# Optimization experiments

Measured on AMD Instinct MI355X. Metric: run time of the kernel, lower is better.

The kernel has to match this reference:

```python
import jax, jax.numpy as jnp
import numpy as np
import math

D_MODEL = 512
NHEAD = 8
D_HEAD = D_MODEL // NHEAD
D_FF = 2048
N_LAYERS = 6
B, S = 8, 2048
EPS = 1e-5


def _layernorm(x, g, b):
    mu = jnp.mean(x, axis=-1, keepdims=True)
    var = jnp.mean(jnp.square(x - mu), axis=-1, keepdims=True)
    return (x - mu) * jax.lax.rsqrt(var + EPS) * g + b


def setup_inputs() -> dict:
    key = jax.random.key(0)
    ks = jax.random.split(key, 10)
    sc = 1.0 / math.sqrt(D_MODEL)
    scf = 1.0 / math.sqrt(D_FF)
    return {
        "x": jax.random.normal(ks[0], (B, S, D_MODEL), jnp.float32),
        "wq": jax.random.normal(ks[1], (N_LAYERS, D_MODEL, D_MODEL), jnp.float32) * sc,
        "wk": jax.random.normal(ks[2], (N_LAYERS, D_MODEL, D_MODEL), jnp.float32) * sc,
        "wv": jax.random.normal(ks[3], (N_LAYERS, D_MODEL, D_MODEL), jnp.float32) * sc,
        "wo": jax.random.normal(ks[4], (N_LAYERS, D_MODEL, D_MODEL), jnp.float32) * sc,
        "w1": jax.random.normal(ks[5], (N_LAYERS, D_MODEL, D_FF), jnp.float32) * sc,
        "b1": jnp.zeros((N_LAYERS, D_FF), jnp.float32),
        "w2": jax.random.normal(ks[6], (N_LAYERS, D_FF, D_MODEL), jnp.float32) * scf,
        "b2": jnp.zeros((N_LAYERS, D_MODEL), jnp.float32),
        "g1": jnp.ones((N_LAYERS, D_MODEL), jnp.float32),
        "beta1": jnp.zeros((N_LAYERS, D_MODEL), jnp.float32),
        "g2": jnp.ones((N_LAYERS, D_MODEL), jnp.float32),
        "beta2": jnp.zeros((N_LAYERS, D_MODEL), jnp.float32),
    }


def reference(x, wq, wk, wv, wo, w1, b1, w2, b2, g1, beta1, g2, beta2):
    scale = 1.0 / math.sqrt(D_HEAD)
    for i in range(N_LAYERS):
        # NOTE: faithful to torch .view(B, nhead, -1, d_head) WITHOUT transpose
        q = (x @ wq[i]).reshape(B, NHEAD, S, D_HEAD)
        k = (x @ wk[i]).reshape(B, NHEAD, S, D_HEAD)
        v = (x @ wv[i]).reshape(B, NHEAD, S, D_HEAD)
        u = jnp.einsum("bhsd,bhtd->bhst", q, k) * scale
        attn = jax.nn.softmax(u, axis=-1)
        o = jnp.einsum("bhst,bhtd->bhsd", attn, v).reshape(B, S, D_MODEL)
        x = _layernorm(x + o @ wo[i], g1[i], beta1[i])
        f = jax.nn.relu(x @ w1[i] + b1[i]) @ w2[i] + b2[i]
        x = _layernorm(x + f, g2[i], beta2[i])
    return x
```

## Files before the change

kernel.cpp:

```cpp
#include <hip/hip_runtime.h>
#include <hip/hip_bf16.h>
#include <stdint.h>

typedef __bf16 bf16_t;
typedef bf16_t bf16x8 __attribute__((ext_vector_type(8)));
typedef bf16_t bf16x4 __attribute__((ext_vector_type(4)));
typedef float  f32x4  __attribute__((ext_vector_type(4)));

#define AS1 __attribute__((address_space(1)))
#define AS3 __attribute__((address_space(3)))

__device__ __forceinline__ void gload_lds16(const void* g, void* l) {
  __builtin_amdgcn_global_load_lds((const AS1 void*)g, (AS3 void*)l, 16, 0, 0);
}

__device__ __forceinline__ float fast_exp2(float x) {
#if __has_builtin(__builtin_amdgcn_exp2f)
  return __builtin_amdgcn_exp2f(x);
#else
  return exp2f(x);
#endif
}

#define QSCALE 0.1803368801111204f

template <int RELU, int BIAS, int QKV, int DBUF>
__global__ __launch_bounds__(256) void gemm_bt(const bf16_t* __restrict__ A,
                                               const bf16_t* __restrict__ Bt,
                                               const float* __restrict__ bias,
                                               bf16_t* __restrict__ Cv,
                                               int M, int N, int K, int ldc) {
  __shared__ __align__(16) char smem[DBUF ? 65536 : 32768];
  const int t = threadIdx.x;
  const int l = t & 63;
  const int w = t >> 6;
  const int wm = w >> 1, wn = w & 1;
  const int lr = l & 15, lg = l >> 4;

  const int gx = gridDim.x;
  const int nwg = gx * gridDim.y;
  const int orig = blockIdx.y * gx + blockIdx.x;
  const int swz = (orig & 7) * (nwg >> 3) + (orig >> 3);
  const long m0 = (long)(swz / gx) * 128;
  const long n0 = (long)(swz % gx) * 128;

  const bf16_t* asrc[4];
  const bf16_t* bsrc[4];
#pragma unroll
  for (int it = 0; it < 4; ++it) {
    int y = it * 4096 + t * 16;
    int row = y >> 7;
    int col = ((y & 127) ^ ((row & 7) << 4)) >> 1;
    asrc[it] = A + (m0 + row) * (long)K + col;
    bsrc[it] = Bt + (n0 + row) * (long)K + col;
  }

  auto stage = [&](int buf) {
    char* sb = smem + buf * 32768;
#pragma unroll
    for (int it = 0; it < 4; ++it) {
      gload_lds16(asrc[it], sb + it * 4096 + t * 16);
      gload_lds16(bsrc[it], sb + 16384 + it * 4096 + t * 16);
      asrc[it] += 64;
      bsrc[it] += 64;
    }
  };

  f32x4 acc[4][4] = {};
  const int nt = K >> 6;

  auto compute = [&](char* sb) {
#pragma unroll
    for (int kk = 0; kk < 2; ++kk) {
      const int c2 = (kk * 32 + lg * 8) * 2;
      bf16x8 a[4], b[4];
#pragma unroll
      for (int i = 0; i < 4; ++i) {
        int ra = wm * 64 + i * 16 + lr;
        a[i] = *(const bf16x8*)(sb + ((ra * 128 + c2) ^ ((ra & 7) << 4)));
        int rb = wn * 64 + i * 16 + lr;
        b[i] = *(const bf16x8*)(sb + 16384 + ((rb * 128 + c2) ^ ((rb & 7) << 4)));
      }
      __builtin_amdgcn_s_setprio(1);
#pragma unroll
      for (int i = 0; i < 4; ++i)
#pragma unroll
        for (int j = 0; j < 4; ++j)
          acc[i][j] = __builtin_amdgcn_mfma_f32_16x16x32_bf16(a[i], b[j], acc[i][j], 0, 0, 0);
      __builtin_amdgcn_s_setprio(0);
    }
  };

  if (DBUF) {
    stage(0);
    __syncthreads();
    int buf = 0;
    for (int kt = 0; kt < nt; ++kt) {
      if (kt + 1 < nt) stage(buf ^ 1);
      compute(smem + buf * 32768);
      __syncthreads();
      buf ^= 1;
    }
  } else {
    for (int kt = 0; kt < nt; ++kt) {
      __syncthreads();
      stage(0);
      __syncthreads();
      compute(smem);
    }
  }

  float bv[4];
  if (BIAS) {
#pragma unroll
    for (int j = 0; j < 4; ++j) bv[j] = bias[n0 + wn * 64 + j * 16 + lr];
  }
#pragma unroll
  for (int i = 0; i < 4; ++i) {
    long rowb = m0 + wm * 64 + i * 16 + lg * 4;
#pragma unroll
    for (int j = 0; j < 4; ++j) {
      int colbase = (int)n0 + wn * 64 + j * 16;
      bf16_t* outp;
      int coll;
      if (QKV) {
        outp = Cv + (size_t)(colbase >> 9) * 8388608;
        coll = (colbase & 511) + lr;
      } else {
        outp = Cv;
        coll = colbase + lr;
      }
#pragma unroll
      for (int r = 0; r < 4; ++r) {
        float v = acc[i][j][r];
        if (BIAS) v += bv[j];
        if (RELU) v = v > 0.f ? v : 0.f;
        outp[(rowb + r) * (long)ldc + coll] = (bf16_t)v;
      }
    }
  }
}

__global__ __launch_bounds__(256) void attn_fa(const bf16_t* __restrict__ qg,
                                               const bf16_t* __restrict__ kg,
                                               const bf16_t* __restrict__ vg,
                                               bf16_t* __restrict__ og) {
  __shared__ __align__(16) char smem[49152];
  const int t = threadIdx.x, l = t & 63, w = t >> 6;
  const int lr = l & 15, lg = l >> 4;
  const int lin = blockIdx.x;
  const int swz = (lin & 7) * 128 + (lin >> 3);
  const long hoff = (long)(swz >> 4) * 131072;
  const int q0 = (swz & 15) * 128 + w * 32;
  const uint32_t LDSB = (uint32_t)(uintptr_t)(AS3 char*)smem;

  bf16x8 qf[2][2];
#pragma unroll
  for (int nf = 0; nf < 2; ++nf)
#pragma unroll
    for (int kk = 0; kk < 2; ++kk)
      qf[nf][kk] = *(const bf16x8*)(qg + hoff + (long)(q0 + nf * 16 + lr) * 64 + kk * 32 + lg * 8);

  const bf16_t* ksrc[2];
#pragma unroll
  for (int i = 0; i < 2; ++i) {
    int y = i * 4096 + t * 16;
    int row = y >> 7;
    int col = ((y & 127) ^ ((row & 7) << 4)) >> 1;
    ksrc[i] = kg + hoff + (long)row * 64 + col;
  }
  const bf16_t* vsrc[2];
#pragma unroll
  for (int i = 0; i < 2; ++i) {
    int y = i * 4096 + t * 16;
    int kk = y >> 12;
    int nj = (y >> 10) & 3;
    int jhi = (y >> 9) & 1;
    int lgs = (y >> 7) & 3;
    int r = (y >> 5) & 3;
    int ch = (y >> 4) & 1;
    int kv = kk * 32 + jhi * 16 + lgs * 4 + r;
    int d0 = nj * 16 + ch * 8;
    vsrc[i] = vg + hoff + (long)kv * 64 + d0;
  }

  auto stage = [&](int buf) {
    char* sb = smem + buf * 16384;
    gload_lds16(ksrc[0], sb + t * 16);
    gload_lds16(ksrc[1], sb + 4096 + t * 16);
    gload_lds16(vsrc[0], sb + 8192 + t * 16);
    gload_lds16(vsrc[1], sb + 12288 + t * 16);
    ksrc[0] += 4096; ksrc[1] += 4096; vsrc[0] += 4096; vsrc[1] += 4096;
  };

  f32x4 oacc[2][4] = {};
  f32x4 lacc[2] = {};
  bf16x8 onesf;
#pragma unroll
  for (int j = 0; j < 8; ++j) onesf[j] = (bf16_t)1.0f;

  stage(0);
  stage(1);
  int cur = 0, nxt = 2;
  for (int ti = 0; ti < 32; ++ti) {
    if (ti == 31) asm volatile("s_waitcnt vmcnt(0)" ::: "memory");
    else          asm volatile("s_waitcnt vmcnt(4)" ::: "memory");
    asm volatile("s_barrier" ::: "memory");
    if (ti < 30) stage(nxt);
    char* sb = smem + cur * 16384;

    f32x4 sT[4][2] = {};
#pragma unroll
    for (int kk = 0; kk < 2; ++kk) {
      const int c2 = (kk * 32 + lg * 8) * 2;
      bf16x8 kf[4];
#pragma unroll
      for (int mf = 0; mf < 4; ++mf) {
        int rk = mf * 16 + lr;
        kf[mf] = *(const bf16x8*)(sb + ((rk * 128 + c2) ^ ((rk & 7) << 4)));
      }
      __builtin_amdgcn_s_setprio(1);
#pragma unroll
      for (int mf = 0; mf < 4; ++mf)
#pragma unroll
        for (int nf = 0; nf < 2; ++nf)
          sT[mf][nf] = __builtin_amdgcn_mfma_f32_16x16x32_bf16(kf[mf], qf[nf][kk], sT[mf][nf], 0, 0, 0);
      __builtin_amdgcn_s_setprio(0);
    }

    uint32_t va = LDSB + (uint32_t)cur * 16384u + 8192u + (uint32_t)l * 8u;
    bf16x4 tv0, tv1, tv2, tv3, tv4, tv5, tv6, tv7;
    bf16x4 tv8, tv9, tva, tvb, tvc, tvd, tve, tvf;
    asm volatile(
        "ds_read_b64_tr_b16 %0, %16 offset:0\n\t"
        "ds_read_b64_tr_b16 %1, %16 offset:512\n\t"
        "ds_read_b64_tr_b16 %2, %16 offset:1024\n\t"
        "ds_read_b64_tr_b16 %3, %16 offset:1536\n\t"
        "ds_read_b64_tr_b16 %4, %16 offset:2048\n\t"
        "ds_read_b64_tr_b16 %5, %16 offset:2560\n\t"
        "ds_read_b64_tr_b16 %6, %16 offset:3072\n\t"
        "ds_read_b64_tr_b16 %7, %16 offset:3584\n\t"
        "ds_read_b64_tr_b16 %8, %16 offset:4096\n\t"
        "ds_read_b64_tr_b16 %9, %16 offset:4608\n\t"
        "ds_read_b64_tr_b16 %10, %16 offset:5120\n\t"
        "ds_read_b64_tr_b16 %11, %16 offset:5632\n\t"
        "ds_read_b64_tr_b16 %12, %16 offset:6144\n\t"
        "ds_read_b64_tr_b16 %13, %16 offset:6656\n\t"
        "ds_read_b64_tr_b16 %14, %16 offset:7168\n\t"
        "ds_read_b64_tr_b16 %15, %16 offset:7680"
        : "=&v"(tv0), "=&v"(tv1), "=&v"(tv2), "=&v"(tv3),
          "=&v"(tv4), "=&v"(tv5), "=&v"(tv6), "=&v"(tv7),
          "=&v"(tv8), "=&v"(tv9), "=&v"(tva), "=&v"(tvb),
          "=&v"(tvc), "=&v"(tvd), "=&v"(tve), "=&v"(tvf)
        : "v"(va));

    bf16x8 pa[2][2];
#pragma unroll
    for (int m2 = 0; m2 < 2; ++m2)
#pragma unroll
      for (int kk = 0; kk < 2; ++kk) {
        f32x4 e0, e1;
#pragma unroll
        for (int r = 0; r < 4; ++r) {
          e0[r] = fast_exp2(sT[2 * kk][m2][r]);
          e1[r] = fast_exp2(sT[2 * kk + 1][m2][r]);
        }
        bf16x4 c0 = __builtin_convertvector(e0, bf16x4);
        bf16x4 c1 = __builtin_convertvector(e1, bf16x4);
        pa[m2][kk] = __builtin_shufflevector(c0, c1, 0, 1, 2, 3, 4, 5, 6, 7);
      }

    asm volatile("s_waitcnt lgkmcnt(0)" ::: "memory");
    __builtin_amdgcn_sched_barrier(0);

    bf16x8 vf[2][4];
    vf[0][0] = __builtin_shufflevector(tv0, tv1, 0, 1, 2, 3, 4, 5, 6, 7);
    vf[0][1] = __builtin_shufflevector(tv2, tv3, 0, 1, 2, 3, 4, 5, 6, 7);
    vf[0][2] = __builtin_shufflevector(tv4, tv5, 0, 1, 2, 3, 4, 5, 6, 7);
    vf[0][3] = __builtin_shufflevector(tv6, tv7, 0, 1, 2, 3, 4, 5, 6, 7);
    vf[1][0] = __builtin_shufflevector(tv8, tv9, 0, 1, 2, 3, 4, 5, 6, 7);
    vf[1][1] = __builtin_shufflevector(tva, tvb, 0, 1, 2, 3, 4, 5, 6, 7);
    vf[1][2] = __builtin_shufflevector(tvc, tvd, 0, 1, 2, 3, 4, 5, 6, 7);
    vf[1][3] = __builtin_shufflevector(tve, tvf, 0, 1, 2, 3, 4, 5, 6, 7);

    __builtin_amdgcn_s_setprio(1);
#pragma unroll
    for (int kk = 0; kk < 2; ++kk)
#pragma unroll
      for (int m2 = 0; m2 < 2; ++m2) {
#pragma unroll
        for (int nj = 0; nj < 4; ++nj)
          oacc[m2][nj] = __builtin_amdgcn_mfma_f32_16x16x32_bf16(pa[m2][kk], vf[kk][nj], oacc[m2][nj], 0, 0, 0);
        lacc[m2] = __builtin_amdgcn_mfma_f32_16x16x32_bf16(pa[m2][kk], onesf, lacc[m2], 0, 0, 0);
      }
    __builtin_amdgcn_s_setprio(0);

    cur = (cur == 2) ? 0 : cur + 1;
    nxt = (nxt == 2) ? 0 : nxt + 1;
  }

#pragma unroll
  for (int m2 = 0; m2 < 2; ++m2)
#pragma unroll
    for (int r = 0; r < 4; ++r) {
      float inv = 1.f / lacc[m2][r];
      long row = q0 + m2 * 16 + lg * 4 + r;
#pragma unroll
      for (int nj = 0; nj < 4; ++nj)
        og[hoff + row * 64 + nj * 16 + lr] = (bf16_t)(oacc[m2][nj][r] * inv);
    }
}

__global__ __launch_bounds__(256) void transpose_w(const float* __restrict__ src,
                                                   bf16_t* __restrict__ dst,
                                                   int K, int N,
                                                   long dstLayerStride, float scale) {
  __shared__ float tile[32][33];
  const int t = threadIdx.x;
  const int tx = t & 31, ty = t >> 5;
  const long ls = (long)blockIdx.z * K * N;
  const long ld = (long)blockIdx.z * dstLayerStride;
  const int n0 = blockIdx.x * 32, k0 = blockIdx.y * 32;
#pragma unroll
  for (int i = 0; i < 4; ++i)
    tile[ty + i * 8][tx] = src[ls + (long)(k0 + ty + i * 8) * N + n0 + tx];
  __syncthreads();
#pragma unroll
  for (int i = 0; i < 4; ++i)
    dst[ld + (long)(n0 + ty + i * 8) * K + k0 + tx] = (bf16_t)(tile[tx][ty + i * 8] * scale);
}

__global__ __launch_bounds__(256) void init_x(const float* __restrict__ x,
                                              bf16_t* __restrict__ xb) {
  long i = ((long)blockIdx.x * 256 + threadIdx.x) * 8;
  f32x4 a = *(const f32x4*)(x + i);
  f32x4 b = *(const f32x4*)(x + i + 4);
  bf16x8 o;
#pragma unroll
  for (int j = 0; j < 4; ++j) { o[j] = (bf16_t)a[j]; o[4 + j] = (bf16_t)b[j]; }
  *(bf16x8*)(xb + i) = o;
}

template <int FINAL>
__global__ __launch_bounds__(256) void resid_ln(const bf16_t* __restrict__ delta,
                                                bf16_t* __restrict__ xb,
                                                float* __restrict__ xout,
                                                const float* __restrict__ g,
                                                const float* __restrict__ b) {
  const int t = threadIdx.x, l = t & 63, w = t >> 6;
  const long row = (long)blockIdx.x * 4 + w;
  const long base = row * 512 + l * 8;
  bf16x8 xv = *(const bf16x8*)(xb + base);
  bf16x8 dv = *(const bf16x8*)(delta + base);
  float s[8];
  float sum = 0.f, sq = 0.f;
#pragma unroll
  for (int j = 0; j < 8; ++j) {
    s[j] = (float)xv[j] + (float)dv[j];
    sum += s[j];
    sq += s[j] * s[j];
  }
#pragma unroll
  for (int m = 1; m <= 32; m <<= 1) {
    sum += __shfl_xor(sum, m, 64);
    sq += __shfl_xor(sq, m, 64);
  }
  float mu = sum * (1.f / 512.f);
  float var = sq * (1.f / 512.f) - mu * mu;
  float rstd = rsqrtf(var + 1e-5f);
  f32x4 g0 = *(const f32x4*)(g + l * 8);
  f32x4 g1v = *(const f32x4*)(g + l * 8 + 4);
  f32x4 b0 = *(const f32x4*)(b + l * 8);
  f32x4 b1v = *(const f32x4*)(b + l * 8 + 4);
  f32x4 y0, y1;
  bf16x8 yb;
#pragma unroll
  for (int j = 0; j < 4; ++j) {
    y0[j] = (s[j] - mu) * rstd * g0[j] + b0[j];
    y1[j] = (s[4 + j] - mu) * rstd * g1v[j] + b1v[j];
    yb[j] = (bf16_t)y0[j];
    yb[4 + j] = (bf16_t)y1[j];
  }
  *(bf16x8*)(xb + base) = yb;
  if (FINAL) {
    *(f32x4*)(xout + base) = y0;
    *(f32x4*)(xout + base + 4) = y1;
  }
}

extern "C" void kernel_launch(void* const* d_in, const int* in_sizes, int n_in,
                              void* d_out, int out_size, void* d_ws, size_t ws_size,
                              hipStream_t stream) {
  const float* x = (const float*)d_in[0];
  const float* wq = (const float*)d_in[1];
  const float* wk = (const float*)d_in[2];
  const float* wv = (const float*)d_in[3];
  const float* wo = (const float*)d_in[4];
  const float* w1 = (const float*)d_in[5];
  const float* b1 = (const float*)d_in[6];
  const float* w2 = (const float*)d_in[7];
  const float* b2 = (const float*)d_in[8];
  const float* g1 = (const float*)d_in[9];
  const float* be1 = (const float*)d_in[10];
  const float* g2 = (const float*)d_in[11];
  const float* be2 = (const float*)d_in[12];

  char* ws = (char*)d_ws;

  const int M = 16384, D = 512, DFF = 2048, NL = 6;
  const size_t sz_small = (size_t)NL * D * D * 2;
  const size_t sz_big = (size_t)NL * D * DFF * 2;
  bf16_t* wqkvt = (bf16_t*)(ws);
  bf16_t* wot = (bf16_t*)(ws + 3 * sz_small);
  bf16_t* w1t = (bf16_t*)(ws + 4 * sz_small);
  bf16_t* w2t = (bf16_t*)(ws + 4 * sz_small + sz_big);
  char* actbase = ws + 4 * sz_small + 2 * sz_big;
  bf16_t* xb = (bf16_t*)(actbase);
  char* R = actbase + (size_t)M * D * 2;
  bf16_t* qb = (bf16_t*)(R);
  bf16_t* kb = (bf16_t*)(R + (size_t)M * D * 2);
  bf16_t* vb = (bf16_t*)(R + 2 * (size_t)M * D * 2);
  bf16_t* ob = (bf16_t*)(R + 3 * (size_t)M * D * 2);
  bf16_t* hb = (bf16_t*)(R);
  bf16_t* tmpb = (bf16_t*)(R + 4 * (size_t)M * D * 2);

  const long LQKV = 1536L * 512;
  transpose_w<<<dim3(D / 32, D / 32, NL), 256, 0, stream>>>(wq, wqkvt, D, D, LQKV, QSCALE);
  transpose_w<<<dim3(D / 32, D / 32, NL), 256, 0, stream>>>(wk, wqkvt + 512 * 512, D, D, LQKV, 1.f);
  transpose_w<<<dim3(D / 32, D / 32, NL), 256, 0, stream>>>(wv, wqkvt + 2 * 512 * 512, D, D, LQKV, 1.f);
  transpose_w<<<dim3(D / 32, D / 32, NL), 256, 0, stream>>>(wo, wot, D, D, (long)D * D, 1.f);
  transpose_w<<<dim3(DFF / 32, D / 32, NL), 256, 0, stream>>>(w1, w1t, D, DFF, (long)D * DFF, 1.f);
  transpose_w<<<dim3(D / 32, DFF / 32, NL), 256, 0, stream>>>(w2, w2t, DFF, D, (long)D * DFF, 1.f);
  init_x<<<4096, 256, 0, stream>>>(x, xb);

  for (int L = 0; L < NL; ++L) {
    const bf16_t* wqkvL = wqkvt + (size_t)L * LQKV;
    const bf16_t* woL = wot + (size_t)L * D * D;
    const bf16_t* w1L = w1t + (size_t)L * D * DFF;
    const bf16_t* w2L = w2t + (size_t)L * D * DFF;

    gemm_bt<0, 0, 1, 0><<<dim3(12, 128), 256, 0, stream>>>(xb, wqkvL, nullptr, qb, M, 1536, D, 512);
    attn_fa<<<dim3(1024), 256, 0, stream>>>(qb, kb, vb, ob);
    gemm_bt<0, 0, 0, 1><<<dim3(4, 128), 256, 0, stream>>>(ob, woL, nullptr, tmpb, M, D, D, D);
    resid_ln<0><<<4096, 256, 0, stream>>>(tmpb, xb, nullptr, g1 + L * D, be1 + L * D);
    gemm_bt<1, 1, 0, 0><<<dim3(16, 128), 256, 0, stream>>>(xb, w1L, b1 + (size_t)L * DFF, hb, M, DFF, D, DFF);
    gemm_bt<0, 1, 0, 1><<<dim3(4, 128), 256, 0, stream>>>(hb, w2L, b2 + L * D, tmpb, M, D, DFF, D);
    if (L == NL - 1)
      resid_ln<1><<<4096, 256, 0, stream>>>(tmpb, xb, (float*)d_out, g2 + L * D, be2 + L * D);
    else
      resid_ln<0><<<4096, 256, 0, stream>>>(tmpb, xb, nullptr, g2 + L * D, be2 + L * D);
  }
}
```

Baseline: 1.482 ms.

## Load K tiles directly into registers and stage only V through LDS

The attention kernel now reads K fragments straight from global memory into registers, double-buffered across iterations, instead of staging K through shared memory. Only V still goes through LDS, so shared memory per block shrinks from 48KB to 16KB with double buffering replacing the triple-buffered ring. This is meant to cut LDS traffic and footprint and allow more blocks per CU. In exchange it raises register pressure from holding two K fragment sets, and each lane now issues its own global K loads. The wait now drains all outstanding memory loads every iteration, which reduces how far prefetch can run ahead.

```diff
diff --git a/kernel.cpp b/kernel.cpp
--- a/kernel.cpp
+++ b/kernel.cpp
@@ -145,7 +145,7 @@
                                                const bf16_t* __restrict__ kg,
                                                const bf16_t* __restrict__ vg,
                                                bf16_t* __restrict__ og) {
-  __shared__ __align__(16) char smem[49152];
+  __shared__ __align__(16) char smem[16384];
   const int t = threadIdx.x, l = t & 63, w = t >> 6;
   const int lr = l & 15, lg = l >> 4;
   const int lin = blockIdx.x;
@@ -161,37 +161,17 @@
     for (int kk = 0; kk < 2; ++kk)
       qf[nf][kk] = *(const bf16x8*)(qg + hoff + (long)(q0 + nf * 16 + lr) * 64 + kk * 32 + lg * 8);
 
-  const bf16_t* ksrc[2];
-#pragma unroll
-  for (int i = 0; i < 2; ++i) {
-    int y = i * 4096 + t * 16;
-    int row = y >> 7;
-    int col = ((y & 127) ^ ((row & 7) << 4)) >> 1;
-    ksrc[i] = kg + hoff + (long)row * 64 + col;
-  }
-  const bf16_t* vsrc[2];
-#pragma unroll
-  for (int i = 0; i < 2; ++i) {
-    int y = i * 4096 + t * 16;
-    int kk = y >> 12;
+  const bf16_t* kbase = kg + hoff + (long)lr * 64 + lg * 8;
+  const bf16_t* vs;
+  {
+    int y = t * 16;
     int nj = (y >> 10) & 3;
     int jhi = (y >> 9) & 1;
     int lgs = (y >> 7) & 3;
     int r = (y >> 5) & 3;
     int ch = (y >> 4) & 1;
-    int kv = kk * 32 + jhi * 16 + lgs * 4 + r;
-    int d0 = nj * 16 + ch * 8;
-    vsrc[i] = vg + hoff + (long)kv * 64 + d0;
-  }
-
-  auto stage = [&](int buf) {
-    char* sb = smem + buf * 16384;
-    gload_lds16(ksrc[0], sb + t * 16);
-    gload_lds16(ksrc[1], sb + 4096 + t * 16);
-    gload_lds16(vsrc[0], sb + 8192 + t * 16);
-    gload_lds16(vsrc[1], sb + 12288 + t * 16);
-    ksrc[0] += 4096; ksrc[1] += 4096; vsrc[0] += 4096; vsrc[1] += 4096;
-  };
+    vs = vg + hoff + (long)(jhi * 16 + lgs * 4 + r) * 64 + nj * 16 + ch * 8;
+  }
 
   f32x4 oacc[2][4] = {};
   f32x4 lacc[2] = {};
@@ -199,36 +179,27 @@
 #pragma unroll
   for (int j = 0; j < 8; ++j) onesf[j] = (bf16_t)1.0f;
 
-  stage(0);
-  stage(1);
-  int cur = 0, nxt = 2;
-  for (int ti = 0; ti < 32; ++ti) {
-    if (ti == 31) asm volatile("s_waitcnt vmcnt(0)" ::: "memory");
-    else          asm volatile("s_waitcnt vmcnt(4)" ::: "memory");
+  bf16x8 kA[2][4], kB[2][4];
+
+  gload_lds16(vs, smem + t * 16);
+  gload_lds16(vs + 2048, smem + 4096 + t * 16);
+  vs += 4096;
+#pragma unroll
+  for (int kk = 0; kk < 2; ++kk)
+#pragma unroll
+    for (int mf = 0; mf < 4; ++mf)
+      kA[kk][mf] = *(const bf16x8*)(kbase + mf * 1024 + kk * 32);
+  kbase += 4096;
+
+  auto iter = [&](int buf, bf16x8 (&kf)[2][4], bool pre, int nbuf, bf16x8 (&kn)[2][4]) {
+    asm volatile("s_waitcnt vmcnt(0)" ::: "memory");
     asm volatile("s_barrier" ::: "memory");
-    if (ti < 30) stage(nxt);
-    char* sb = smem + cur * 16384;
-
-    f32x4 sT[4][2] = {};
-#pragma unroll
-    for (int kk = 0; kk < 2; ++kk) {
-      const int c2 = (kk * 32 + lg * 8) * 2;
-      bf16x8 kf[4];
-#pragma unroll
-      for (int mf = 0; mf < 4; ++mf) {
-        int rk = mf * 16 + lr;
-        kf[mf] = *(const bf16x8*)(sb + ((rk * 128 + c2) ^ ((rk & 7) << 4)));
-      }
-      __builtin_amdgcn_s_setprio(1);
-#pragma unroll
-      for (int mf = 0; mf < 4; ++mf)
-#pragma unroll
-        for (int nf = 0; nf < 2; ++nf)
-          sT[mf][nf] = __builtin_amdgcn_mfma_f32_16x16x32_bf16(kf[mf], qf[nf][kk], sT[mf][nf], 0, 0, 0);
-      __builtin_amdgcn_s_setprio(0);
-    }
-
-    uint32_t va = LDSB + (uint32_t)cur * 16384u + 8192u + (uint32_t)l * 8u;
+    if (pre) {
+      gload_lds16(vs, smem + nbuf * 8192 + t * 16);
+      gload_lds16(vs + 2048, smem + nbuf * 8192 + 4096 + t * 16);
+      vs += 4096;
+    }
+    uint32_t va = LDSB + (uint32_t)buf * 8192u + (uint32_t)l * 8u;
     bf16x4 tv0, tv1, tv2, tv3, tv4, tv5, tv6, tv7;
     bf16x4 tv8, tv9, tva, tvb, tvc, tvd, tve, tvf;
     asm volatile(
@@ -253,6 +224,25 @@
           "=&v"(tv8), "=&v"(tv9), "=&v"(tva), "=&v"(tvb),
           "=&v"(tvc), "=&v"(tvd), "=&v"(tve), "=&v"(tvf)
         : "v"(va));
+    if (pre) {
+#pragma unroll
+      for (int kk = 0; kk < 2; ++kk)
+#pragma unroll
+        for (int mf = 0; mf < 4; ++mf)
+          kn[kk][mf] = *(const bf16x8*)(kbase + mf * 1024 + kk * 32);
+      kbase += 4096;
+    }
+
+    f32x4 sT[4][2] = {};
+    __builtin_amdgcn_s_setprio(1);
+#pragma unroll
+    for (int kk = 0; kk < 2; ++kk)
+#pragma unroll
+      for (int mf = 0; mf < 4; ++mf)
+#pragma unroll
+        for (int nf = 0; nf < 2; ++nf)
+          sT[mf][nf] = __builtin_amdgcn_mfma_f32_16x16x32_bf16(kf[kk][mf], qf[nf][kk], sT[mf][nf], 0, 0, 0);
+    __builtin_amdgcn_s_setprio(0);
 
     bf16x8 pa[2][2];
 #pragma unroll
@@ -294,9 +284,12 @@
         lacc[m2] = __builtin_amdgcn_mfma_f32_16x16x32_bf16(pa[m2][kk], onesf, lacc[m2], 0, 0, 0);
       }
     __builtin_amdgcn_s_setprio(0);
-
-    cur = (cur == 2) ? 0 : cur + 1;
-    nxt = (nxt == 2) ? 0 : nxt + 1;
+  };
+
+  for (int ti = 0; ti < 32; ti += 2) {
+    iter(0, kA, true, 1, kB);
+    bool more = (ti + 2 < 32);
+    iter(1, kB, more, 0, kA);
   }
 
 #pragma unroll
```

Result: slower. 2.113 ms (+42.5%).

## Fuse output-projection and FFN2 GEMMs with residual add and LayerNorm

Applied to the files above, without the earlier changes.

Replaces the Wo and W2 GEMMs plus their separate resid_ln kernels with one gemm_resln kernel. Each 512-thread block computes a full 64x512 row tile, so the LayerNorm reduction can finish in-block through LDS. This drops the bf16 temporary round trip and two launches per layer. The cost is that only 256 blocks run, using about 144KB of LDS each, which lowers parallelism and occupancy. The epilogue also does scalar, uncoalesced loads and stores of xb.

```diff
diff --git a/kernel.cpp b/kernel.cpp
--- a/kernel.cpp
+++ b/kernel.cpp
@@ -139,6 +139,156 @@
       }
     }
   }
+}
+
+template <int BIAS, int FINAL>
+__global__ __launch_bounds__(512) void gemm_resln(const bf16_t* __restrict__ A,
+                                                  const bf16_t* __restrict__ Bt,
+                                                  const float* __restrict__ bias,
+                                                  bf16_t* __restrict__ xb,
+                                                  float* __restrict__ xout,
+                                                  const float* __restrict__ g,
+                                                  const float* __restrict__ be,
+                                                  int K) {
+  __shared__ __align__(16) char smem[147456];
+  const int t = threadIdx.x, l = t & 63, w = t >> 6;
+  const int lr = l & 15, lg = l >> 4;
+  const int orig = blockIdx.x;
+  const int swz = (orig & 7) * 32 + (orig >> 3);
+  const long m0 = (long)swz * 64;
+
+  const bf16_t* src[9];
+#pragma unroll
+  for (int i = 0; i < 9; ++i) {
+    int gy = i * 8192 + t * 16;
+    if (gy < 8192) {
+      int row = gy >> 7;
+      int col = ((gy & 127) ^ ((row & 7) << 4)) >> 1;
+      src[i] = A + (m0 + row) * (long)K + col;
+    } else {
+      int by = gy - 8192;
+      int row = by >> 7;
+      int col = ((by & 127) ^ ((row & 7) << 4)) >> 1;
+      src[i] = Bt + (long)row * K + col;
+    }
+  }
+  auto stage = [&](int buf) {
+    char* sb = smem + buf * 73728;
+#pragma unroll
+    for (int i = 0; i < 9; ++i) {
+      gload_lds16(src[i], sb + i * 8192 + t * 16);
+      src[i] += 64;
+    }
+  };
+
+  f32x4 acc[4][4] = {};
+  const int nt = K >> 6;
+  stage(0);
+  __syncthreads();
+  int buf = 0;
+  for (int kt = 0; kt < nt; ++kt) {
+    if (kt + 1 < nt) stage(buf ^ 1);
+    char* sb = smem + buf * 73728;
+#pragma unroll
+    for (int kk = 0; kk < 2; ++kk) {
+      const int c2 = (kk * 32 + lg * 8) * 2;
+      bf16x8 a[4], b[4];
+#pragma unroll
+      for (int i = 0; i < 4; ++i) {
+        int ra = i * 16 + lr;
+        a[i] = *(const bf16x8*)(sb + ((ra * 128 + c2) ^ ((ra & 7) << 4)));
+        int rb = w * 64 + i * 16 + lr;
+        b[i] = *(const bf16x8*)(sb + 8192 + ((rb * 128 + c2) ^ ((rb & 7) << 4)));
+      }
+      __builtin_amdgcn_s_setprio(1);
+#pragma unroll
+      for (int i = 0; i < 4; ++i)
+#pragma unroll
+        for (int j = 0; j < 4; ++j)
+          acc[i][j] = __builtin_amdgcn_mfma_f32_16x16x32_bf16(a[i], b[j], acc[i][j], 0, 0, 0);
+      __builtin_amdgcn_s_setprio(0);
+    }
+    __syncthreads();
+    buf ^= 1;
+  }
+
+  float* lnsum = (float*)smem;
+  float* lnsq  = (float*)(smem + 2048);
+  float* lnm   = (float*)(smem + 4096);
+  float* lnr   = (float*)(smem + 4352);
+
+  float bv[4];
+  if (BIAS) {
+#pragma unroll
+    for (int j = 0; j < 4; ++j) bv[j] = bias[w * 64 + j * 16 + lr];
+  }
+  float sv[4][4][4];
+#pragma unroll
+  for (int i = 0; i < 4; ++i)
+#pragma unroll
+    for (int r = 0; r < 4; ++r) {
+      long row = m0 + i * 16 + lg * 4 + r;
+#pragma unroll
+      for (int j = 0; j < 4; ++j) {
+        float d = acc[i][j][r];
+        if (BIAS) d += bv[j];
+        float xold = (float)xb[row * 512 + w * 64 + j * 16 + lr];
+        sv[i][r][j] = xold + d;
+      }
+    }
+#pragma unroll
+  for (int i = 0; i < 4; ++i)
+#pragma unroll
+    for (int r = 0; r < 4; ++r) {
+      float ps = sv[i][r][0] + sv[i][r][1] + sv[i][r][2] + sv[i][r][3];
+      float pq = sv[i][r][0] * sv[i][r][0] + sv[i][r][1] * sv[i][r][1] +
+                 sv[i][r][2] * sv[i][r][2] + sv[i][r][3] * sv[i][r][3];
+#pragma unroll
+      for (int m = 1; m <= 8; m <<= 1) {
+        ps += __shfl_xor(ps, m, 64);
+        pq += __shfl_xor(pq, m, 64);
+      }
+      if (lr == 0) {
+        int rl = i * 16 + lg * 4 + r;
+        lnsum[rl * 8 + w] = ps;
+        lnsq[rl * 8 + w] = pq;
+      }
+    }
+  __syncthreads();
+  if (t < 64) {
+    float s8 = 0.f, q8 = 0.f;
+#pragma unroll
+    for (int wv = 0; wv < 8; ++wv) {
+      s8 += lnsum[t * 8 + wv];
+      q8 += lnsq[t * 8 + wv];
+    }
+    float mu = s8 * (1.f / 512.f);
+    float var = q8 * (1.f / 512.f) - mu * mu;
+    lnm[t] = mu;
+    lnr[t] = rsqrtf(var + 1e-5f);
+  }
+  __syncthreads();
+  float gv[4], bev[4];
+#pragma unroll
+  for (int j = 0; j < 4; ++j) {
+    gv[j] = g[w * 64 + j * 16 + lr];
+    bev[j] = be[w * 64 + j * 16 + lr];
+  }
+#pragma unroll
+  for (int i = 0; i < 4; ++i)
+#pragma unroll
+    for (int r = 0; r < 4; ++r) {
+      int rl = i * 16 + lg * 4 + r;
+      long row = m0 + rl;
+      float mu = lnm[rl], rstd = lnr[rl];
+#pragma unroll
+      for (int j = 0; j < 4; ++j) {
+        int col = w * 64 + j * 16 + lr;
+        float y = (sv[i][r][j] - mu) * rstd * gv[j] + bev[j];
+        xb[row * 512 + col] = (bf16_t)y;
+        if (FINAL) xout[row * 512 + col] = y;
+      }
+    }
 }
 
 __global__ __launch_bounds__(256) void attn_fa(const bf16_t* __restrict__ qg,
@@ -341,53 +491,6 @@
   *(bf16x8*)(xb + i) = o;
 }
 
-template <int FINAL>
-__global__ __launch_bounds__(256) void resid_ln(const bf16_t* __restrict__ delta,
-                                                bf16_t* __restrict__ xb,
-                                                float* __restrict__ xout,
-                                                const float* __restrict__ g,
-                                                const float* __restrict__ b) {
-  const int t = threadIdx.x, l = t & 63, w = t >> 6;
-  const long row = (long)blockIdx.x * 4 + w;
-  const long base = row * 512 + l * 8;
-  bf16x8 xv = *(const bf16x8*)(xb + base);
-  bf16x8 dv = *(const bf16x8*)(delta + base);
-  float s[8];
-  float sum = 0.f, sq = 0.f;
-#pragma unroll
-  for (int j = 0; j < 8; ++j) {
-    s[j] = (float)xv[j] + (float)dv[j];
-    sum += s[j];
-    sq += s[j] * s[j];
-  }
-#pragma unroll
-  for (int m = 1; m <= 32; m <<= 1) {
-    sum += __shfl_xor(sum, m, 64);
-    sq += __shfl_xor(sq, m, 64);
-  }
-  float mu = sum * (1.f / 512.f);
-  float var = sq * (1.f / 512.f) - mu * mu;
-  float rstd = rsqrtf(var + 1e-5f);
-  f32x4 g0 = *(const f32x4*)(g + l * 8);
-  f32x4 g1v = *(const f32x4*)(g + l * 8 + 4);
-  f32x4 b0 = *(const f32x4*)(b + l * 8);
-  f32x4 b1v = *(const f32x4*)(b + l * 8 + 4);
-  f32x4 y0, y1;
-  bf16x8 yb;
-#pragma unroll
-  for (int j = 0; j < 4; ++j) {
-    y0[j] = (s[j] - mu) * rstd * g0[j] + b0[j];
-    y1[j] = (s[4 + j] - mu) * rstd * g1v[j] + b1v[j];
-    yb[j] = (bf16_t)y0[j];
-    yb[4 + j] = (bf16_t)y1[j];
-  }
-  *(bf16x8*)(xb + base) = yb;
-  if (FINAL) {
-    *(f32x4*)(xout + base) = y0;
-    *(f32x4*)(xout + base + 4) = y1;
-  }
-}
-
 extern "C" void kernel_launch(void* const* d_in, const int* in_sizes, int n_in,
                               void* d_out, int out_size, void* d_ws, size_t ws_size,
                               hipStream_t stream) {
@@ -422,7 +525,6 @@
   bf16_t* vb = (bf16_t*)(R + 2 * (size_t)M * D * 2);
   bf16_t* ob = (bf16_t*)(R + 3 * (size_t)M * D * 2);
   bf16_t* hb = (bf16_t*)(R);
-  bf16_t* tmpb = (bf16_t*)(R + 4 * (size_t)M * D * 2);
 
   const long LQKV = 1536L * 512;
   transpose_w<<<dim3(D / 32, D / 32, NL), 256, 0, stream>>>(wq, wqkvt, D, D, LQKV, QSCALE);
@@ -441,13 +543,14 @@
 
     gemm_bt<0, 0, 1, 0><<<dim3(12, 128), 256, 0, stream>>>(xb, wqkvL, nullptr, qb, M, 1536, D, 512);
     attn_fa<<<dim3(1024), 256, 0, stream>>>(qb, kb, vb, ob);
-    gemm_bt<0, 0, 0, 1><<<dim3(4, 128), 256, 0, stream>>>(ob, woL, nullptr, tmpb, M, D, D, D);
-    resid_ln<0><<<4096, 256, 0, stream>>>(tmpb, xb, nullptr, g1 + L * D, be1 + L * D);
+    gemm_resln<0, 0><<<dim3(256), 512, 0, stream>>>(ob, woL, nullptr, xb, nullptr,
+                                                    g1 + L * D, be1 + L * D, D);
     gemm_bt<1, 1, 0, 0><<<dim3(16, 128), 256, 0, stream>>>(xb, w1L, b1 + (size_t)L * DFF, hb, M, DFF, D, DFF);
-    gemm_bt<0, 1, 0, 1><<<dim3(4, 128), 256, 0, stream>>>(hb, w2L, b2 + L * D, tmpb, M, D, DFF, D);
     if (L == NL - 1)
-      resid_ln<1><<<4096, 256, 0, stream>>>(tmpb, xb, (float*)d_out, g2 + L * D, be2 + L * D);
+      gemm_resln<1, 1><<<dim3(256), 512, 0, stream>>>(hb, w2L, b2 + L * D, xb, (float*)d_out,
+                                                      g2 + L * D, be2 + L * D, DFF);
     else
-      resid_ln<0><<<4096, 256, 0, stream>>>(tmpb, xb, nullptr, g2 + L * D, be2 + L * D);
-  }
-}
+      gemm_resln<1, 0><<<dim3(256), 512, 0, stream>>>(hb, w2L, b2 + L * D, xb, nullptr,
+                                                      g2 + L * D, be2 + L * D, DFF);
+  }
+}
```

Measured after the change: 1.487 ms. About the same (+0.3%).
